# Kernel optimization log

Measured on AMD Instinct MI355X. Metric: run time of the kernel, lower is better.

Reference implementation:

```python
import jax, jax.numpy as jnp
import numpy as np

EMBED_DIM = 1024
NUM_HEADS = 16
HEAD_DIM = EMBED_DIM // NUM_HEADS


def setup_inputs() -> dict:
    key = jax.random.key(0)
    ks = jax.random.split(key, 12)
    B, S, D = 4, 2048, EMBED_DIM
    scale = 1.0 / np.sqrt(D)
    inp = {
        "query": jax.random.normal(ks[0], (B, S, D), jnp.float32),
        "key": jax.random.normal(ks[1], (B, S, D), jnp.float32),
        "value": jax.random.normal(ks[2], (B, S, D), jnp.float32),
        # nn.Linear weights: [out_features, in_features], y = x @ W.T + b
        "Wq": jax.random.normal(ks[3], (D, D), jnp.float32) * scale,
        "bq": jnp.zeros((D,), jnp.float32),
        "Wk": jax.random.normal(ks[4], (D, D), jnp.float32) * scale,
        "bk": jnp.zeros((D,), jnp.float32),
        "Wv": jax.random.normal(ks[5], (D, D), jnp.float32) * scale,
        "bv": jnp.zeros((D,), jnp.float32),
        "Wo": jax.random.normal(ks[6], (D, D), jnp.float32) * scale,
        "bo": jnp.zeros((D,), jnp.float32),
    }
    return inp


def reference(query, key, value, Wq, bq, Wk, bk, Wv, bv, Wo, bo):
    B, Sq, D = query.shape
    Sk = key.shape[1]
    H, Dh = NUM_HEADS, HEAD_DIM

    def proj(x, W, b):
        # [B,S,D] -> [B,H,S,Dh]
        y = jnp.einsum('bsd,ed->bse', x, W) + b
        return y.reshape(x.shape[0], x.shape[1], H, Dh).transpose(0, 2, 1, 3)

    q = proj(query, Wq, bq)
    k = proj(key, Wk, bk)
    v = proj(value, Wv, bv)

    # sigmoid attention (no softmax); dropout is identity in eval mode
    scores = jnp.einsum('bhqd,bhkd->bhqk', q, k) / jnp.sqrt(jnp.float32(Dh)).astype(q.dtype)
    attn = jax.nn.sigmoid(scores)
    out = jnp.einsum('bhqk,bhkd->bhqd', attn, v)

    out = out.transpose(0, 2, 1, 3).reshape(B, Sq, D)
    return jnp.einsum('bsd,ed->bse', out, Wo) + bo
```

## Files before the change

kernel.cpp:

```cpp
#include <hip/hip_runtime.h>


typedef _Float16 f16x4 __attribute__((ext_vector_type(4)));
typedef _Float16 f16x8 __attribute__((ext_vector_type(8)));
typedef float    f32x4 __attribute__((ext_vector_type(4)));
typedef float    f32x16 __attribute__((ext_vector_type(16)));

typedef __attribute__((address_space(3))) void* lds_vp;
typedef const __attribute__((address_space(1))) void* gbl_vp;

__device__ __forceinline__ void gld_lds16(const void* g, void* l) {
  __builtin_amdgcn_global_load_lds((gbl_vp)g, (lds_vp)l, 16, 0, 0);
}

__device__ __forceinline__ f16x8 cvt8(float4 a, float4 b) {
  return (f16x8){(_Float16)a.x, (_Float16)a.y, (_Float16)a.z, (_Float16)a.w,
                 (_Float16)b.x, (_Float16)b.y, (_Float16)b.z, (_Float16)b.w};
}

#define BM 128
#define BN 128
#define BK 32


template <bool AF16, bool BF16, bool TRANSV, bool OUTF32>
__global__ __launch_bounds__(256) void gemm_bt(const void* __restrict__ Av,
                                               const void* __restrict__ Bv,
                                               const float* __restrict__ bias,
                                               void* __restrict__ Yv,
                                               int M, int N, int K) {
  __shared__ __align__(16) _Float16 sA[BM * BK];
  __shared__ __align__(16) _Float16 sB[BN * BK];

  const int t = threadIdx.x, lane = t & 63, wid = t >> 6;
  const int m0 = blockIdx.x * BM, n0 = blockIdx.y * BN;
  const int wm = (wid >> 1) * 64, wn = (wid & 1) * 64;
  const int lrow = lane & 15, g = lane >> 4;

  f32x4 acc[4][4] = {};

  const int arow = 16 * wid + (lane >> 2);
  const int gq = (lane & 3) ^ ((lane >> 3) & 3);
  _Float16* lA1 = sA + wid * 512;
  _Float16* lA2 = sA + 2048 + wid * 512;
  _Float16* lB1 = sB + wid * 512;
  _Float16* lB2 = sB + 2048 + wid * 512;

  const int mrow = t >> 1, mhalf = t & 1;
  const int mm = (mrow >> 1) & 3;
  const int ch_lo = mrow * 4 + ((2 * mhalf) ^ mm);
  const int ch_hi = ch_lo ^ 1;

  const _Float16* pA16a = nullptr; const _Float16* pA16b = nullptr;
  const float* pA32 = nullptr;
  if constexpr (AF16) {
    const _Float16* A = (const _Float16*)Av;
    pA16a = A + (size_t)(m0 + arow) * K + gq * 8;
    pA16b = A + (size_t)(m0 + 64 + arow) * K + gq * 8;
  } else {
    pA32 = (const float*)Av + (size_t)(m0 + mrow) * K + mhalf * 16;
  }
  const _Float16* pB16a = nullptr; const _Float16* pB16b = nullptr;
  const float* pB32 = nullptr;
  if constexpr (BF16) {
    const _Float16* B = (const _Float16*)Bv;
    pB16a = B + (size_t)(n0 + arow) * K + gq * 8;
    pB16b = B + (size_t)(n0 + 64 + arow) * K + gq * 8;
  } else {
    pB32 = (const float*)Bv + (size_t)(n0 + mrow) * K + mhalf * 16;
  }

  const int xr = g ^ ((lrow >> 1) & 3);

  for (int k0 = 0; k0 < K; k0 += BK) {
    float4 av[4], bv4[4];
    if constexpr (!AF16) {
      const float4* p = (const float4*)(pA32 + k0);
      av[0] = p[0]; av[1] = p[1]; av[2] = p[2]; av[3] = p[3];
    }
    if constexpr (!BF16) {
      const float4* p = (const float4*)(pB32 + k0);
      bv4[0] = p[0]; bv4[1] = p[1]; bv4[2] = p[2]; bv4[3] = p[3];
    }
    __syncthreads();
    if constexpr (AF16) {
      gld_lds16(pA16a + k0, lA1);
      gld_lds16(pA16b + k0, lA2);
    } else {
      *(f16x8*)(sA + ch_lo * 8) = cvt8(av[0], av[1]);
      *(f16x8*)(sA + ch_hi * 8) = cvt8(av[2], av[3]);
    }
    if constexpr (BF16) {
      gld_lds16(pB16a + k0, lB1);
      gld_lds16(pB16b + k0, lB2);
    } else {
      *(f16x8*)(sB + ch_lo * 8) = cvt8(bv4[0], bv4[1]);
      *(f16x8*)(sB + ch_hi * 8) = cvt8(bv4[2], bv4[3]);
    }
    __syncthreads();

    f16x8 af[4], bf[4];
#pragma unroll
    for (int i = 0; i < 4; i++)
      af[i] = *(const f16x8*)(sA + (wm + i * 16 + lrow) * 32 + xr * 8);
#pragma unroll
    for (int j = 0; j < 4; j++)
      bf[j] = *(const f16x8*)(sB + (wn + j * 16 + lrow) * 32 + xr * 8);
#pragma unroll
    for (int i = 0; i < 4; i++)
#pragma unroll
      for (int j = 0; j < 4; j++)
        acc[i][j] = __builtin_amdgcn_mfma_f32_16x16x32_f16(af[i], bf[j], acc[i][j], 0, 0, 0);
  }

  const int orow = g * 4, ocol = lrow;
#pragma unroll
  for (int j = 0; j < 4; j++) {
    const int col = n0 + wn + j * 16 + ocol;
    const float bv = bias[col];
#pragma unroll
    for (int i = 0; i < 4; i++) {
      const int row = m0 + wm + i * 16 + orow;
      if constexpr (TRANSV) {
        _Float16* VT = (_Float16*)Yv;
        int s = row & 2047;
        int sp = (s & ~12) | ((s & 4) << 1) | ((s & 8) >> 1);
        _Float16* dst = VT + (((size_t)(row >> 11) * 16 + (col >> 6)) * 64 + (col & 63)) * 2048 + sp;
        f16x4 v = {(_Float16)(acc[i][j][0] + bv), (_Float16)(acc[i][j][1] + bv),
                   (_Float16)(acc[i][j][2] + bv), (_Float16)(acc[i][j][3] + bv)};
        *(f16x4*)dst = v;
      } else if constexpr (OUTF32) {
        float* Y = (float*)Yv;
#pragma unroll
        for (int r = 0; r < 4; r++) Y[(size_t)(row + r) * N + col] = acc[i][j][r] + bv;
      } else {
        _Float16* Y = (_Float16*)Yv;
#pragma unroll
        for (int r = 0; r < 4; r++) Y[(size_t)(row + r) * N + col] = (_Float16)(acc[i][j][r] + bv);
      }
    }
  }
}

__global__ __launch_bounds__(256) void qkv_gemm(const _Float16* __restrict__ Xq,
                                                const _Float16* __restrict__ Xk,
                                                const _Float16* __restrict__ Xv,
                                                const _Float16* __restrict__ W,
                                                const float* __restrict__ bq,
                                                const float* __restrict__ bk,
                                                const float* __restrict__ bv,
                                                _Float16* __restrict__ Qo,
                                                _Float16* __restrict__ Ko,
                                                _Float16* __restrict__ VT) {
  __shared__ __align__(16) _Float16 sA[BM * BK];
  __shared__ __align__(16) _Float16 sB[BN * BK];

  const int t = threadIdx.x, lane = t & 63, wid = t >> 6;
  const int n0g = blockIdx.x * BN, m0 = blockIdx.y * BM;
  const int seg = blockIdx.x >> 3, n0 = n0g & 1023;
  const _Float16* A = (seg == 0) ? Xq : (seg == 1) ? Xk : Xv;
  const float* bias = (seg == 0) ? bq : (seg == 1) ? bk : bv;
  const int K = 1024;

  const int wm = (wid >> 1) * 64, wn = (wid & 1) * 64;
  const int lrow = lane & 15, g = lane >> 4;

  f32x4 acc[4][4] = {};

  const int arow = 16 * wid + (lane >> 2);
  const int gq = (lane & 3) ^ ((lane >> 3) & 3);
  _Float16* lA1 = sA + wid * 512;
  _Float16* lA2 = sA + 2048 + wid * 512;
  _Float16* lB1 = sB + wid * 512;
  _Float16* lB2 = sB + 2048 + wid * 512;

  const _Float16* pA16a = A + (size_t)(m0 + arow) * K + gq * 8;
  const _Float16* pA16b = A + (size_t)(m0 + 64 + arow) * K + gq * 8;
  const _Float16* pB16a = W + (size_t)(n0g + arow) * K + gq * 8;
  const _Float16* pB16b = W + (size_t)(n0g + 64 + arow) * K + gq * 8;

  const int xr = g ^ ((lrow >> 1) & 3);

  for (int k0 = 0; k0 < K; k0 += BK) {
    __syncthreads();
    gld_lds16(pA16a + k0, lA1);
    gld_lds16(pA16b + k0, lA2);
    gld_lds16(pB16a + k0, lB1);
    gld_lds16(pB16b + k0, lB2);
    __syncthreads();

    f16x8 af[4], bf[4];
#pragma unroll
    for (int i = 0; i < 4; i++)
      af[i] = *(const f16x8*)(sA + (wm + i * 16 + lrow) * 32 + xr * 8);
#pragma unroll
    for (int j = 0; j < 4; j++)
      bf[j] = *(const f16x8*)(sB + (wn + j * 16 + lrow) * 32 + xr * 8);
#pragma unroll
    for (int i = 0; i < 4; i++)
#pragma unroll
      for (int j = 0; j < 4; j++)
        acc[i][j] = __builtin_amdgcn_mfma_f32_16x16x32_f16(af[i], bf[j], acc[i][j], 0, 0, 0);
  }

  const int orow = g * 4, ocol = lrow;
#pragma unroll
  for (int j = 0; j < 4; j++) {
    const int col = n0 + wn + j * 16 + ocol;
    const float bvv = bias[col];
#pragma unroll
    for (int i = 0; i < 4; i++) {
      const int row = m0 + wm + i * 16 + orow;
      if (seg == 2) {
        int s = row & 2047;
        int sp = (s & ~12) | ((s & 4) << 1) | ((s & 8) >> 1);
        _Float16* dst = VT + (((size_t)(row >> 11) * 16 + (col >> 6)) * 64 + (col & 63)) * 2048 + sp;
        f16x4 v = {(_Float16)(acc[i][j][0] + bvv), (_Float16)(acc[i][j][1] + bvv),
                   (_Float16)(acc[i][j][2] + bvv), (_Float16)(acc[i][j][3] + bvv)};
        *(f16x4*)dst = v;
      } else {
        _Float16* Y = (seg == 0) ? Qo : Ko;
#pragma unroll
        for (int r = 0; r < 4; r++) Y[(size_t)(row + r) * 1024 + col] = (_Float16)(acc[i][j][r] + bvv);
      }
    }
  }
}

#define LDS_ROW 72

__global__ __launch_bounds__(256, 2) void attn_sig(const _Float16* __restrict__ Q,
                                                   const _Float16* __restrict__ K,
                                                   const _Float16* __restrict__ VT,
                                                   _Float16* __restrict__ O) {
  __shared__ __align__(16) _Float16 smem[256 * LDS_ROW];
  _Float16* sK = smem;
  _Float16* sVT = smem + 64 * LDS_ROW;

  const int t = threadIdx.x, lane = t & 63, wid = t >> 6;
  const int l31 = lane & 31, g5 = lane >> 5;
  const int b = blockIdx.z, h = blockIdx.y, q0 = blockIdx.x * 256;
  const int qw = q0 + wid * 64;

  f16x8 qf[2][4];
#pragma unroll
  for (int qt = 0; qt < 2; qt++) {
    const _Float16* qp = Q + (size_t)(b * 2048 + qw + qt * 32 + l31) * 1024 + h * 64;
#pragma unroll
    for (int dhc = 0; dhc < 4; dhc++) qf[qt][dhc] = *(const f16x8*)(qp + dhc * 16 + g5 * 8);
  }

  f32x16 oacc[2][2] = {};

  const int srow = t >> 2, scol = (t & 3) * 16;
  const _Float16* kbase = K + ((size_t)(b * 2048) + srow) * 1024 + h * 64 + scol;
  const _Float16* vbase = VT + ((size_t)((b * 16 + h) * 64 + srow)) * 2048 + scol;

  for (int kt = 0; kt < 2048; kt += 64) {
    uint4 ka = *(const uint4*)(kbase + (size_t)kt * 1024);
    uint4 kb = *(const uint4*)(kbase + (size_t)kt * 1024 + 8);
    uint4 va = *(const uint4*)(vbase + kt);
    uint4 vb = *(const uint4*)(vbase + kt + 8);
    __syncthreads();
    *(uint4*)&sK[srow * LDS_ROW + scol] = ka;
    *(uint4*)&sK[srow * LDS_ROW + scol + 8] = kb;
    *(uint4*)&sVT[srow * LDS_ROW + scol] = va;
    *(uint4*)&sVT[srow * LDS_ROW + scol + 8] = vb;
    __syncthreads();

#pragma unroll
    for (int kt32 = 0; kt32 < 2; kt32++) {
      f16x8 kf[4];
#pragma unroll
      for (int dhc = 0; dhc < 4; dhc++)
        kf[dhc] = *(const f16x8*)&sK[(kt32 * 32 + l31) * LDS_ROW + dhc * 16 + g5 * 8];

      f16x4 p16[2][4];
#pragma unroll
      for (int qt = 0; qt < 2; qt++) {
        f32x16 sacc = {};
#pragma unroll
        for (int dhc = 0; dhc < 4; dhc++)
          sacc = __builtin_amdgcn_mfma_f32_32x32x16_f16(kf[dhc], qf[qt][dhc], sacc, 0, 0, 0);
#pragma unroll
        for (int c = 0; c < 4; c++) {
          f16x4 p4;
#pragma unroll
          for (int r = 0; r < 4; r++) {
            float e = __expf(sacc[4 * c + r] * -0.125f);
            p4[r] = (_Float16)__builtin_amdgcn_rcpf(1.0f + e);
          }
          p16[qt][c] = p4;
        }
      }

#pragma unroll
      for (int dht = 0; dht < 2; dht++)
#pragma unroll
        for (int tloc = 0; tloc < 2; tloc++) {
          f16x8 vfr = *(const f16x8*)&sVT[(dht * 32 + l31) * LDS_ROW + kt32 * 32 + tloc * 16 + g5 * 8];
          f16x4 vlo = __builtin_shufflevector(vfr, vfr, 0, 1, 2, 3);
          f16x4 vhi = __builtin_shufflevector(vfr, vfr, 4, 5, 6, 7);
#pragma unroll
          for (int qt = 0; qt < 2; qt++) {
            oacc[qt][dht] = __builtin_amdgcn_mfma_f32_32x32x8f16(vlo, p16[qt][tloc * 2 + 0],
                                                                 oacc[qt][dht], 0, 0, 0);
            oacc[qt][dht] = __builtin_amdgcn_mfma_f32_32x32x8f16(vhi, p16[qt][tloc * 2 + 1],
                                                                 oacc[qt][dht], 0, 0, 0);
          }
        }
    }
  }

  __syncthreads();
  _Float16* ep = smem;
#pragma unroll
  for (int qt = 0; qt < 2; qt++)
#pragma unroll
    for (int dht = 0; dht < 2; dht++)
#pragma unroll
      for (int c = 0; c < 4; c++) {
        f16x4 o4 = {(_Float16)oacc[qt][dht][4 * c + 0], (_Float16)oacc[qt][dht][4 * c + 1],
                    (_Float16)oacc[qt][dht][4 * c + 2], (_Float16)oacc[qt][dht][4 * c + 3]};
        *(f16x4*)&ep[(wid * 64 + qt * 32 + l31) * LDS_ROW + dht * 32 + c * 8 + g5 * 4] = o4;
      }
  __syncthreads();
#pragma unroll
  for (int i = 0; i < 8; i++) {
    const int q = i * 32 + (t >> 3), dhc = t & 7;
    f16x8 row = *(const f16x8*)&ep[q * LDS_ROW + dhc * 8];
    *(f16x8*)(O + (size_t)(b * 2048 + q0 + q) * 1024 + h * 64 + dhc * 8) = row;
  }
}

struct CvtArgs {
  const float* src[7];
  _Float16* dst[7];
  int n[7];
  int cnt;
};

__global__ __launch_bounds__(256) void cvt_f32_f16(CvtArgs a) {
  const int ti = blockIdx.y;
  if (ti >= a.cnt) return;
  const int i = (blockIdx.x * 256 + threadIdx.x) * 8;
  if (i >= a.n[ti]) return;
  const float4* s = (const float4*)(a.src[ti] + i);
  float4 x = s[0], y = s[1];
  *(f16x8*)(a.dst[ti] + i) = cvt8(x, y);
}

extern "C" void kernel_launch(void* const* d_in, const int* in_sizes, int n_in,
                              void* d_out, int out_size, void* d_ws, size_t ws_size,
                              hipStream_t stream) {
  const float* query = (const float*)d_in[0];
  const float* key   = (const float*)d_in[1];
  const float* value = (const float*)d_in[2];
  const float* Wq = (const float*)d_in[3];
  const float* bq = (const float*)d_in[4];
  const float* Wk = (const float*)d_in[5];
  const float* bk = (const float*)d_in[6];
  const float* Wv = (const float*)d_in[7];
  const float* bv = (const float*)d_in[8];
  const float* Wo = (const float*)d_in[9];
  const float* bo = (const float*)d_in[10];
  float* out = (float*)d_out;

  const int D = 1024, M = 8192;
  const size_t MB = 1024 * 1024;
  char* ws = (char*)d_ws;
  dim3 bb(256), ga(8, 16, 4);

  if (ws_size >= 104 * MB) {
    _Float16* Xq = (_Float16*)(ws + 0 * MB);
    _Float16* Xk = (_Float16*)(ws + 16 * MB);
    _Float16* Xv = (_Float16*)(ws + 32 * MB);
    _Float16* Qp = (_Float16*)(ws + 48 * MB);
    _Float16* Kp = (_Float16*)(ws + 64 * MB);
    _Float16* VT = (_Float16*)(ws + 80 * MB);
    _Float16* Wf = (_Float16*)(ws + 96 * MB);
    _Float16* AO = Xq;
    CvtArgs ca{};
    ca.src[0] = query; ca.dst[0] = Xq; ca.n[0] = M * D;
    ca.src[1] = key;   ca.dst[1] = Xk; ca.n[1] = M * D;
    ca.src[2] = value; ca.dst[2] = Xv; ca.n[2] = M * D;
    ca.src[3] = Wq; ca.dst[3] = Wf + 0 * 1048576; ca.n[3] = D * D;
    ca.src[4] = Wk; ca.dst[4] = Wf + 1 * 1048576; ca.n[4] = D * D;
    ca.src[5] = Wv; ca.dst[5] = Wf + 2 * 1048576; ca.n[5] = D * D;
    ca.src[6] = Wo; ca.dst[6] = Wf + 3 * 1048576; ca.n[6] = D * D;
    ca.cnt = 7;
    cvt_f32_f16<<<dim3(4096, 7), bb, 0, stream>>>(ca);
    qkv_gemm<<<dim3(24, 64), bb, 0, stream>>>(Xq, Xk, Xv, Wf, bq, bk, bv, Qp, Kp, VT);
    attn_sig<<<ga, bb, 0, stream>>>(Qp, Kp, VT, AO);
    gemm_bt<true, true, false, true><<<dim3(64, 8), bb, 0, stream>>>(AO, Wf + 3 * 1048576, bo, out, M, D, D);
  } else {
    _Float16* Qp = (_Float16*)(ws + 0 * MB);
    _Float16* Kp = (_Float16*)(ws + 16 * MB);
    _Float16* VT = (_Float16*)(ws + 32 * MB);
    _Float16* AO = (_Float16*)(ws + 48 * MB);
    gemm_bt<false, false, false, false><<<dim3(64, 8), bb, 0, stream>>>(query, Wq, bq, Qp, M, D, D);
    gemm_bt<false, false, false, false><<<dim3(64, 8), bb, 0, stream>>>(key,   Wk, bk, Kp, M, D, D);
    gemm_bt<false, false, true,  false><<<dim3(64, 8), bb, 0, stream>>>(value, Wv, bv, VT, M, D, D);
    attn_sig<<<ga, bb, 0, stream>>>(Qp, Kp, VT, AO);
    gemm_bt<true, false, false, true><<<dim3(64, 8), bb, 0, stream>>>(AO, Wo, bo, out, M, D, D);
  }
}
```

Measured before the change: 379.5 us.

## Shrink attention tile to 128 queries, prefetch K/V, fold scale into Q

Each attention block now covers 128 queries with 32 per wave instead of 256 with 64. This halves register and LDS use so four blocks can share a CU, and doubles the grid. The global loads of the next K/V tile are issued before compute on the current one, as register prefetch. The -1/8 scale is folded into Q up front, sigmoid outputs are packed with cvt_pkrtz, and the PV product uses the 32x32x16 MFMA in place of paired 32x32x8 ones. The risks are that the scale is rounded in fp16 on Q, and each K/V tile is reused across fewer queries, which raises L2 traffic.

```diff
diff --git a/kernel.cpp b/kernel.cpp
--- a/kernel.cpp
+++ b/kernel.cpp
@@ -1,8 +1,10 @@
 #include <hip/hip_runtime.h>
 
 
+typedef _Float16 f16x2 __attribute__((ext_vector_type(2)));
 typedef _Float16 f16x4 __attribute__((ext_vector_type(4)));
 typedef _Float16 f16x8 __attribute__((ext_vector_type(8)));
+typedef __fp16   h16x2 __attribute__((ext_vector_type(2)));
 typedef float    f32x4 __attribute__((ext_vector_type(4)));
 typedef float    f32x16 __attribute__((ext_vector_type(16)));
 
@@ -18,10 +20,14 @@
                  (_Float16)b.x, (_Float16)b.y, (_Float16)b.z, (_Float16)b.w};
 }
 
+__device__ __forceinline__ f16x2 pk2(float a, float b) {
+  h16x2 r = __builtin_amdgcn_cvt_pkrtz(a, b);
+  return __builtin_bit_cast(f16x2, r);
+}
+
 #define BM 128
 #define BN 128
 #define BK 32
-
 
 template <bool AF16, bool BF16, bool TRANSV, bool OUTF32>
 __global__ __launch_bounds__(256) void gemm_bt(const void* __restrict__ Av,
@@ -229,38 +235,39 @@
 
 #define LDS_ROW 72
 
-__global__ __launch_bounds__(256, 2) void attn_sig(const _Float16* __restrict__ Q,
+__global__ __launch_bounds__(256, 4) void attn_sig(const _Float16* __restrict__ Q,
                                                    const _Float16* __restrict__ K,
                                                    const _Float16* __restrict__ VT,
                                                    _Float16* __restrict__ O) {
-  __shared__ __align__(16) _Float16 smem[256 * LDS_ROW];
+  __shared__ __align__(16) _Float16 smem[128 * LDS_ROW];
   _Float16* sK = smem;
   _Float16* sVT = smem + 64 * LDS_ROW;
 
   const int t = threadIdx.x, lane = t & 63, wid = t >> 6;
   const int l31 = lane & 31, g5 = lane >> 5;
-  const int b = blockIdx.z, h = blockIdx.y, q0 = blockIdx.x * 256;
-  const int qw = q0 + wid * 64;
-
-  f16x8 qf[2][4];
-#pragma unroll
-  for (int qt = 0; qt < 2; qt++) {
-    const _Float16* qp = Q + (size_t)(b * 2048 + qw + qt * 32 + l31) * 1024 + h * 64;
-#pragma unroll
-    for (int dhc = 0; dhc < 4; dhc++) qf[qt][dhc] = *(const f16x8*)(qp + dhc * 16 + g5 * 8);
-  }
-
-  f32x16 oacc[2][2] = {};
+  const int b = blockIdx.z, h = blockIdx.y, q0 = blockIdx.x * 128;
+  const int qw = q0 + wid * 32;
+
+  f16x8 qf[4];
+  {
+    const _Float16* qp = Q + (size_t)(b * 2048 + qw + l31) * 1024 + h * 64;
+#pragma unroll
+    for (int dhc = 0; dhc < 4; dhc++)
+      qf[dhc] = *(const f16x8*)(qp + dhc * 16 + g5 * 8) * (_Float16)-0.125f;
+  }
+
+  f32x16 oacc[2] = {};
 
   const int srow = t >> 2, scol = (t & 3) * 16;
   const _Float16* kbase = K + ((size_t)(b * 2048) + srow) * 1024 + h * 64 + scol;
   const _Float16* vbase = VT + ((size_t)((b * 16 + h) * 64 + srow)) * 2048 + scol;
 
+  uint4 ka = *(const uint4*)kbase;
+  uint4 kb = *(const uint4*)(kbase + 8);
+  uint4 va = *(const uint4*)vbase;
+  uint4 vb = *(const uint4*)(vbase + 8);
+
   for (int kt = 0; kt < 2048; kt += 64) {
-    uint4 ka = *(const uint4*)(kbase + (size_t)kt * 1024);
-    uint4 kb = *(const uint4*)(kbase + (size_t)kt * 1024 + 8);
-    uint4 va = *(const uint4*)(vbase + kt);
-    uint4 vb = *(const uint4*)(vbase + kt + 8);
     __syncthreads();
     *(uint4*)&sK[srow * LDS_ROW + scol] = ka;
     *(uint4*)&sK[srow * LDS_ROW + scol + 8] = kb;
@@ -268,6 +275,14 @@
     *(uint4*)&sVT[srow * LDS_ROW + scol + 8] = vb;
     __syncthreads();
 
+    const int kt2 = kt + 64;
+    if (kt2 < 2048) {
+      ka = *(const uint4*)(kbase + (size_t)kt2 * 1024);
+      kb = *(const uint4*)(kbase + (size_t)kt2 * 1024 + 8);
+      va = *(const uint4*)(vbase + kt2);
+      vb = *(const uint4*)(vbase + kt2 + 8);
+    }
+
 #pragma unroll
     for (int kt32 = 0; kt32 < 2; kt32++) {
       f16x8 kf[4];
@@ -275,39 +290,31 @@
       for (int dhc = 0; dhc < 4; dhc++)
         kf[dhc] = *(const f16x8*)&sK[(kt32 * 32 + l31) * LDS_ROW + dhc * 16 + g5 * 8];
 
-      f16x4 p16[2][4];
-#pragma unroll
-      for (int qt = 0; qt < 2; qt++) {
-        f32x16 sacc = {};
-#pragma unroll
-        for (int dhc = 0; dhc < 4; dhc++)
-          sacc = __builtin_amdgcn_mfma_f32_32x32x16_f16(kf[dhc], qf[qt][dhc], sacc, 0, 0, 0);
-#pragma unroll
-        for (int c = 0; c < 4; c++) {
-          f16x4 p4;
-#pragma unroll
-          for (int r = 0; r < 4; r++) {
-            float e = __expf(sacc[4 * c + r] * -0.125f);
-            p4[r] = (_Float16)__builtin_amdgcn_rcpf(1.0f + e);
-          }
-          p16[qt][c] = p4;
+      f32x16 sacc = {};
+#pragma unroll
+      for (int dhc = 0; dhc < 4; dhc++)
+        sacc = __builtin_amdgcn_mfma_f32_32x32x16_f16(kf[dhc], qf[dhc], sacc, 0, 0, 0);
+
+      f16x8 pf[2];
+#pragma unroll
+      for (int G = 0; G < 2; G++) {
+        union { f16x8 v; f16x2 h[4]; } u;
+#pragma unroll
+        for (int pr = 0; pr < 4; pr++) {
+          float e0 = __expf(sacc[G * 8 + pr * 2 + 0]);
+          float e1 = __expf(sacc[G * 8 + pr * 2 + 1]);
+          u.h[pr] = pk2(__builtin_amdgcn_rcpf(1.0f + e0),
+                        __builtin_amdgcn_rcpf(1.0f + e1));
         }
+        pf[G] = u.v;
       }
 
 #pragma unroll
       for (int dht = 0; dht < 2; dht++)
 #pragma unroll
-        for (int tloc = 0; tloc < 2; tloc++) {
-          f16x8 vfr = *(const f16x8*)&sVT[(dht * 32 + l31) * LDS_ROW + kt32 * 32 + tloc * 16 + g5 * 8];
-          f16x4 vlo = __builtin_shufflevector(vfr, vfr, 0, 1, 2, 3);
-          f16x4 vhi = __builtin_shufflevector(vfr, vfr, 4, 5, 6, 7);
-#pragma unroll
-          for (int qt = 0; qt < 2; qt++) {
-            oacc[qt][dht] = __builtin_amdgcn_mfma_f32_32x32x8f16(vlo, p16[qt][tloc * 2 + 0],
-                                                                 oacc[qt][dht], 0, 0, 0);
-            oacc[qt][dht] = __builtin_amdgcn_mfma_f32_32x32x8f16(vhi, p16[qt][tloc * 2 + 1],
-                                                                 oacc[qt][dht], 0, 0, 0);
-          }
+        for (int G = 0; G < 2; G++) {
+          f16x8 vf = *(const f16x8*)&sVT[(dht * 32 + l31) * LDS_ROW + kt32 * 32 + G * 16 + g5 * 8];
+          oacc[dht] = __builtin_amdgcn_mfma_f32_32x32x16_f16(vf, pf[G], oacc[dht], 0, 0, 0);
         }
     }
   }
@@ -315,18 +322,16 @@
   __syncthreads();
   _Float16* ep = smem;
 #pragma unroll
-  for (int qt = 0; qt < 2; qt++)
-#pragma unroll
-    for (int dht = 0; dht < 2; dht++)
-#pragma unroll
-      for (int c = 0; c < 4; c++) {
-        f16x4 o4 = {(_Float16)oacc[qt][dht][4 * c + 0], (_Float16)oacc[qt][dht][4 * c + 1],
-                    (_Float16)oacc[qt][dht][4 * c + 2], (_Float16)oacc[qt][dht][4 * c + 3]};
-        *(f16x4*)&ep[(wid * 64 + qt * 32 + l31) * LDS_ROW + dht * 32 + c * 8 + g5 * 4] = o4;
-      }
+  for (int dht = 0; dht < 2; dht++)
+#pragma unroll
+    for (int c = 0; c < 4; c++) {
+      f16x4 o4 = {(_Float16)oacc[dht][4 * c + 0], (_Float16)oacc[dht][4 * c + 1],
+                  (_Float16)oacc[dht][4 * c + 2], (_Float16)oacc[dht][4 * c + 3]};
+      *(f16x4*)&ep[(wid * 32 + l31) * LDS_ROW + dht * 32 + c * 8 + g5 * 4] = o4;
+    }
   __syncthreads();
 #pragma unroll
-  for (int i = 0; i < 8; i++) {
+  for (int i = 0; i < 4; i++) {
     const int q = i * 32 + (t >> 3), dhc = t & 7;
     f16x8 row = *(const f16x8*)&ep[q * LDS_ROW + dhc * 8];
     *(f16x8*)(O + (size_t)(b * 2048 + q0 + q) * 1024 + h * 64 + dhc * 8) = row;
@@ -369,7 +374,7 @@
   const int D = 1024, M = 8192;
   const size_t MB = 1024 * 1024;
   char* ws = (char*)d_ws;
-  dim3 bb(256), ga(8, 16, 4);
+  dim3 bb(256), ga(16, 16, 4);
 
   if (ws_size >= 104 * MB) {
     _Float16* Xq = (_Float16*)(ws + 0 * MB);
```

Result: no change. 377.3 us (-0.6%).
